# Performance work log

Hardware: AMD Instinct MI355X
Metric: run time of the kernel (lower is better)

Reference implementation:

```python
import jax, jax.numpy as jnp
from jax import lax
import numpy as np

# ---- module hyperparameters (from init_kwargs) ----
DIM = 256
DIM_HEAD = 64
HEADS = 4
GROUPS = 4                      # offset_groups (defaults to heads)
INNER = DIM_HEAD * HEADS        # 256
OFF_DIMS = INNER // GROUPS      # 64
DOWN = 4
KS = 6
PAD = (KS - DOWN) // 2          # 1
OFFSET_SCALE = float(DOWN)      # offset_scale defaults to down_sample_factor
CPB_DIM = DIM // 4              # 64
SCALE = DIM_HEAD ** -0.5


def make_grid(h, w, dtype):
    # torch.meshgrid(arange(w), arange(h), indexing='xy') stacked at dim 0:
    # channel 0 = x (column index), channel 1 = y (row index); shape [2,h,w]
    yy, xx = jnp.meshgrid(jnp.arange(h), jnp.arange(w), indexing='ij')
    return jnp.stack([xx, yy], axis=0).astype(dtype)


def normalize_grid_c(vg):
    # vg: [..., 2, h, w] -> [..., h, w, 2]; faithful to source: channel 0
    # normalized by (h-1), channel 1 by (w-1) (source's h/w naming quirk).
    h, w = vg.shape[-2:]
    gh = 2.0 * vg[..., 0, :, :] / max(h - 1, 1) - 1.0
    gw = 2.0 * vg[..., 1, :, :] / max(w - 1, 1) - 1.0
    return jnp.stack([gh, gw], axis=-1)


def grid_sample_zeros(img, grid):
    # F.grid_sample bilinear, padding_mode='zeros', align_corners=False
    # img: [N,C,H,W]; grid: [N,Hg,Wg,2] with (..,0)=x, (..,1)=y in [-1,1]
    N, C, H, W = img.shape
    ix = ((grid[..., 0] + 1.0) * W - 1.0) * 0.5
    iy = ((grid[..., 1] + 1.0) * H - 1.0) * 0.5
    x0 = jnp.floor(ix)
    y0 = jnp.floor(iy)

    def gather(yy, xx):
        valid = (xx >= 0) & (xx <= W - 1) & (yy >= 0) & (yy <= H - 1)
        xc = jnp.clip(xx, 0, W - 1).astype(jnp.int32)
        yc = jnp.clip(yy, 0, H - 1).astype(jnp.int32)
        vals = jax.vmap(lambda im, y_, x_: im[:, y_, x_])(img, yc, xc)  # [N,C,Hg,Wg]
        return vals * valid[:, None, :, :].astype(img.dtype)

    wa = (x0 + 1 - ix) * (y0 + 1 - iy)
    wb = (ix - x0) * (y0 + 1 - iy)
    wc = (x0 + 1 - ix) * (iy - y0)
    wd = (ix - x0) * (iy - y0)
    return (gather(y0, x0) * wa[:, None]
            + gather(y0, x0 + 1) * wb[:, None]
            + gather(y0 + 1, x0) * wc[:, None]
            + gather(y0 + 1, x0 + 1) * wd[:, None])


def gconv1x1(t, w):
    # grouped 1x1 conv (no bias): t [b, G*Ci, h, w], w [G, Co, Ci]
    G, Co, Ci = w.shape
    bb, _, hh, ww = t.shape
    tg = t.reshape(bb, G, Ci, hh, ww)
    return jnp.einsum('bgihw,goi->bgohw', tg, w).reshape(bb, G * Co, hh, ww)


def setup_inputs() -> dict:
    key = jax.random.key(0)
    ks = jax.random.split(key, 12)
    s = 0.02
    B, H, W = 8, 32, 32
    cg = DIM // GROUPS  # per-group in-channels = 64
    og = INNER // GROUPS  # per-group out-channels = 64
    return {
        'x': jax.random.normal(ks[0], (B, DIM, H, W), jnp.float32),
        'wq': jax.random.normal(ks[1], (GROUPS, og, cg), jnp.float32) * s,
        'wk': jax.random.normal(ks[2], (GROUPS, og, cg), jnp.float32) * s,
        'wv': jax.random.normal(ks[3], (GROUPS, og, cg), jnp.float32) * s,
        'w_off_dw': jax.random.normal(ks[4], (OFF_DIMS, 1, KS, KS), jnp.float32) * s,
        'b_off_dw': jnp.zeros((OFF_DIMS,), jnp.float32),
        'w_off_pw': jax.random.normal(ks[5], (2, OFF_DIMS), jnp.float32) * s,
        'cpb_w1': jax.random.normal(ks[6], (CPB_DIM, 2), jnp.float32) * s,
        'cpb_b1': jnp.zeros((CPB_DIM,), jnp.float32),
        'cpb_w2': jax.random.normal(ks[7], (CPB_DIM, CPB_DIM), jnp.float32) * s,
        'cpb_b2': jnp.zeros((CPB_DIM,), jnp.float32),
        'cpb_w3': jax.random.normal(ks[8], (HEADS // GROUPS, CPB_DIM), jnp.float32) * s,
        'cpb_b3': jnp.zeros((HEADS // GROUPS,), jnp.float32),
        'w_out': jax.random.normal(ks[9], (DIM, INNER), jnp.float32) * s,
        'b_out': jnp.zeros((DIM,), jnp.float32),
    }


def reference(x, wq, wk, wv, w_off_dw, b_off_dw, w_off_pw,
              cpb_w1, cpb_b1, cpb_w2, cpb_b2, cpb_w3, cpb_b3,
              w_out, b_out):
    b, _, H, W = x.shape

    q = gconv1x1(x, wq)                                       # [b, INNER, H, W]
    gq = q.reshape(b * GROUPS, OFF_DIMS, H, W)                # grouped queries
    gx = x.reshape(b * GROUPS, DIM // GROUPS, H, W)           # grouped input

    # to_offsets: depthwise conv -> GELU -> 1x1 conv -> tanh -> scale
    off = lax.conv_general_dilated(
        gq, w_off_dw, window_strides=(DOWN, DOWN),
        padding=[(PAD, PAD), (PAD, PAD)],
        dimension_numbers=('NCHW', 'OIHW', 'NCHW'),
        feature_group_count=OFF_DIMS)
    off = off + b_off_dw[None, :, None, None]
    off = jax.nn.gelu(off, approximate=False)
    off = jnp.einsum('bchw,oc->bohw', off, w_off_pw)
    off = jnp.tanh(off) * OFFSET_SCALE                        # [bg, 2, h2, w2]

    h2, w2 = off.shape[-2:]
    vg = make_grid(h2, w2, off.dtype)[None] + off             # [bg, 2, h2, w2]
    vgs = normalize_grid_c(vg)                                # [bg, h2, w2, 2]

    kv = grid_sample_zeros(gx, vgs)                           # [bg, DIM/G, h2, w2]
    kv = kv.reshape(b, DIM, h2, w2)
    k = gconv1x1(kv, wk)
    v = gconv1x1(kv, wv)
    q = q * SCALE

    def to_heads(t):
        bb, _, hh, ww = t.shape
        return t.reshape(bb, HEADS, DIM_HEAD, hh * ww).transpose(0, 1, 3, 2)

    qh, kh, vh = to_heads(q), to_heads(k), to_heads(v)        # [b, h, i|j, d]
    sim = jnp.einsum('bhid,bhjd->bhij', qh, kh)               # [b, h, HW, h2*w2]

    # CPB relative position bias
    grid_q = normalize_grid_c(make_grid(H, W, x.dtype)).reshape(1, H * W, 2)
    grid_kv = vgs.reshape(b * GROUPS, h2 * w2, 2)
    pos = grid_q[:, :, None, :] - grid_kv[:, None, :, :]      # [bg, i, j, 2]
    bias = jnp.sign(pos) * jnp.log1p(jnp.abs(pos))
    bias = jax.nn.relu(bias @ cpb_w1.T + cpb_b1)
    bias = jax.nn.relu(bias @ cpb_w2.T + cpb_b2)
    bias = bias @ cpb_w3.T + cpb_b3                           # [bg, i, j, o]
    o = HEADS // GROUPS
    bias = bias.reshape(b, GROUPS, H * W, h2 * w2, o)
    bias = bias.transpose(0, 1, 4, 2, 3).reshape(b, HEADS, H * W, h2 * w2)

    attn = jax.nn.softmax(sim + bias, axis=-1)
    out = jnp.einsum('bhij,bhjd->bhid', attn, vh)             # [b, h, HW, d]
    out = out.transpose(0, 1, 3, 2).reshape(b, INNER, H, W)
    out = jnp.einsum('bchw,oc->bohw', out, w_out) + b_out[None, :, None, None]
    return out
```

## Files before the change

kernel.cpp:

```cpp
#include <hip/hip_runtime.h>
#include <hip/hip_bf16.h>
#include <math.h>

#define QSCALE 0.125f

typedef __attribute__((ext_vector_type(8))) short short8b;
typedef __attribute__((ext_vector_type(8))) _Float16 half8;
typedef __attribute__((ext_vector_type(4))) float f32x4;

__device__ __forceinline__ uint pack2(float a, float b) {
    uint r;
    asm("v_cvt_pk_bf16_f32 %0, %1, %2" : "=v"(r) : "v"(a), "v"(b));
    return r;
}
__device__ __forceinline__ uint pkrtz(float a, float b) {
    uint r;
    asm("v_cvt_pkrtz_f16_f32 %0, %1, %2" : "=v"(r) : "v"(a), "v"(b));
    return r;
}
__device__ __forceinline__ uint pk_fma_f16(uint a, uint b, uint c) {
    uint r;
    asm("v_pk_fma_f16 %0, %1, %2, %3" : "=v"(r) : "v"(a), "v"(b), "v"(c));
    return r;
}
__device__ __forceinline__ uint pk_max_f16(uint a, uint b) {
    uint r;
    asm("v_pk_max_f16 %0, %1, %2" : "=v"(r) : "v"(a), "v"(b));
    return r;
}
__device__ __forceinline__ float slogf_(float p) {
    return copysignf(log1pf(fabsf(p)), p);
}

__global__ __launch_bounds__(256) void k_qproj(const float* __restrict__ x,
                                               const float* __restrict__ wq,
                                               float* __restrict__ q,
                                               short* __restrict__ qbt) {
    __shared__ float Wst[64 * 64];
    __shared__ float xs[64 * 128];
    int ht = blockIdx.x, g = blockIdx.y, b = blockIdx.z;
    int tid = threadIdx.x;
    for (int e = tid; e < 4096; e += 256) {
        int co = e >> 6, ci = e & 63;
        Wst[ci * 64 + co] = wq[(g * 64 + co) * 64 + ci];
    }
    const float* xb = x + (b * 256 + g * 64) * 1024 + ht * 128;
    for (int e = tid; e < 2048; e += 256) {
        int ci = e >> 5, hq = e & 31;
        *(float4*)&xs[ci * 128 + hq * 4] = *(const float4*)&xb[ci * 1024 + hq * 4];
    }
    __syncthreads();
    int cg = tid >> 4, hg = tid & 15;
    int co0 = cg * 4, hw0 = hg * 8;
    float acc[4][8];
    for (int a = 0; a < 4; a++) for (int c = 0; c < 8; c++) acc[a][c] = 0.f;
    for (int ci = 0; ci < 64; ci++) {
        float4 a4 = *(float4*)&Wst[ci * 64 + co0];
        float4 b0 = *(float4*)&xs[ci * 128 + hw0];
        float4 b1 = *(float4*)&xs[ci * 128 + hw0 + 4];
        float av[4] = {a4.x, a4.y, a4.z, a4.w};
        float bv[8] = {b0.x, b0.y, b0.z, b0.w, b1.x, b1.y, b1.z, b1.w};
        #pragma unroll
        for (int a = 0; a < 4; a++)
            #pragma unroll
            for (int c = 0; c < 8; c++) acc[a][c] += av[a] * bv[c];
    }
    float* qb = q + (b * 256 + g * 64) * 1024 + ht * 128;
    for (int a = 0; a < 4; a++) {
        float4 o0 = {acc[a][0], acc[a][1], acc[a][2], acc[a][3]};
        float4 o1 = {acc[a][4], acc[a][5], acc[a][6], acc[a][7]};
        *(float4*)&qb[(co0 + a) * 1024 + hw0] = o0;
        *(float4*)&qb[(co0 + a) * 1024 + hw0 + 4] = o1;
    }
    short* q16 = qbt + ((size_t)((b * 4 + g) * 1024 + ht * 128)) * 64;
    for (int c = 0; c < 8; c++) {
        int i = hw0 + c;
        uint2 uu;
        uu.x = pack2(acc[0][c] * QSCALE, acc[1][c] * QSCALE);
        uu.y = pack2(acc[2][c] * QSCALE, acc[3][c] * QSCALE);
        *(uint2*)&q16[i * 64 + co0] = uu;
    }
}

__global__ __launch_bounds__(256) void k_dw(const float* __restrict__ q,
                                            const float* __restrict__ wdw,
                                            const float* __restrict__ bdw,
                                            float* __restrict__ gdw) {
    __shared__ float qs[8 * 1024];
    __shared__ float wds[8 * 36];
    int cg = blockIdx.x, n = blockIdx.y;
    int b = n >> 2, gg = n & 3;
    int c0 = cg * 8;
    int tid = threadIdx.x;
    const float* qn = q + (b * 256 + gg * 64 + c0) * 1024;
    for (int e = tid; e < 2048; e += 256)
        ((float4*)qs)[e] = ((const float4*)qn)[e];
    for (int e = tid; e < 288; e += 256)
        wds[e] = wdw[c0 * 36 + e];
    __syncthreads();
    for (int e = tid; e < 512; e += 256) {
        int c = e >> 6, pos = e & 63;
        int oy = pos >> 3, ox = pos & 7;
        float acc = bdw[c0 + c];
        #pragma unroll
        for (int ky = 0; ky < 6; ky++) {
            int iy = oy * 4 - 1 + ky;
            if (iy < 0 || iy > 31) continue;
            #pragma unroll
            for (int kx = 0; kx < 6; kx++) {
                int ix = ox * 4 - 1 + kx;
                if (ix < 0 || ix > 31) continue;
                acc += qs[c * 1024 + iy * 32 + ix] * wds[c * 36 + ky * 6 + kx];
            }
        }
        gdw[(n * 64 + c0 + c) * 64 + pos] = acc * 0.5f * (1.f + erff(acc * 0.70710678118654752f));
    }
}

__global__ __launch_bounds__(64) void k_pw(const float* __restrict__ gdw,
                                           const float* __restrict__ wpw,
                                           float* __restrict__ vgs) {
    int n = blockIdx.x, pos = threadIdx.x;
    const float* gp = gdw + n * 4096 + pos;
    float a0 = 0.f, a1 = 0.f;
    #pragma unroll 8
    for (int c = 0; c < 64; c++) {
        float v = gp[c * 64];
        a0 += v * wpw[c];
        a1 += v * wpw[64 + c];
    }
    float offx = tanhf(a0) * 4.0f, offy = tanhf(a1) * 4.0f;
    int oy = pos >> 3, ox = pos & 7;
    vgs[(n * 64 + pos) * 2]     = 2.f * ((float)ox + offx) / 7.f - 1.f;
    vgs[(n * 64 + pos) * 2 + 1] = 2.f * ((float)oy + offy) / 7.f - 1.f;
}

__global__ __launch_bounds__(256) void k_sample(const float* __restrict__ x,
                                                const float* __restrict__ vgs,
                                                float* __restrict__ kv) {
    int idx = blockIdx.x * 256 + threadIdx.x;
    int pos = idx & 63, c = (idx >> 6) & 63, n = idx >> 12;
    int b = n >> 2, g = n & 3;
    float gx = vgs[(n * 64 + pos) * 2];
    float gy = vgs[(n * 64 + pos) * 2 + 1];
    float ix = (gx + 1.f) * 16.f - 0.5f;
    float iy = (gy + 1.f) * 16.f - 0.5f;
    float x0 = floorf(ix), y0 = floorf(iy);
    float wa = (x0 + 1.f - ix) * (y0 + 1.f - iy);
    float wb = (ix - x0) * (y0 + 1.f - iy);
    float wc = (x0 + 1.f - ix) * (iy - y0);
    float wd = (ix - x0) * (iy - y0);
    const float* img = x + (b * 256 + g * 64 + c) * 1024;
    int xi = (int)x0, yi = (int)y0;
    float acc = 0.f;
    if (xi >= 0 && xi <= 31 && yi >= 0 && yi <= 31)         acc += img[yi * 32 + xi] * wa;
    if (xi + 1 >= 0 && xi + 1 <= 31 && yi >= 0 && yi <= 31) acc += img[yi * 32 + xi + 1] * wb;
    if (xi >= 0 && xi <= 31 && yi + 1 >= 0 && yi + 1 <= 31) acc += img[(yi + 1) * 32 + xi] * wc;
    if (xi + 1 >= 0 && xi + 1 <= 31 && yi + 1 >= 0 && yi + 1 <= 31) acc += img[(yi + 1) * 32 + xi + 1] * wd;
    kv[(n * 64 + c) * 64 + pos] = acc;
}

__global__ __launch_bounds__(256) void k_kvproj(const float* __restrict__ kv,
                                                const float* __restrict__ wk,
                                                const float* __restrict__ wv,
                                                short* __restrict__ kob,
                                                short* __restrict__ vob) {
    __shared__ float kvs[4096];
    __shared__ float wkt[4096];
    __shared__ float wvt[4096];
    int n = blockIdx.x, g = n & 3;
    int tid = threadIdx.x;
    for (int e = tid; e < 4096; e += 256) {
        int co = e >> 6, ci = e & 63;
        wkt[ci * 64 + co] = wk[(g * 64 + co) * 64 + ci];
        wvt[ci * 64 + co] = wv[(g * 64 + co) * 64 + ci];
        kvs[e] = kv[n * 4096 + e];
    }
    __syncthreads();
    int cg = tid >> 4, jg = tid & 15;
    int co0 = cg * 4, j0 = jg * 4;
    float ak[4][4] = {}, av[4][4] = {};
    for (int ci = 0; ci < 64; ci++) {
        float4 a1 = *(float4*)&wkt[ci * 64 + co0];
        float4 a2 = *(float4*)&wvt[ci * 64 + co0];
        float4 b4 = *(float4*)&kvs[ci * 64 + j0];
        float w1v[4] = {a1.x, a1.y, a1.z, a1.w};
        float w2v[4] = {a2.x, a2.y, a2.z, a2.w};
        float bb[4] = {b4.x, b4.y, b4.z, b4.w};
        #pragma unroll
        for (int a = 0; a < 4; a++)
            #pragma unroll
            for (int j = 0; j < 4; j++) { ak[a][j] += w1v[a] * bb[j]; av[a][j] += w2v[a] * bb[j]; }
    }
    for (int jj = 0; jj < 4; jj++) {
        uint2 uu;
        uu.x = pack2(ak[0][jj], ak[1][jj]);
        uu.y = pack2(ak[2][jj], ak[3][jj]);
        *(uint2*)&kob[n * 4096 + (j0 + jj) * 64 + co0] = uu;
    }
    for (int a = 0; a < 4; a++) {
        uint2 uu;
        uu.x = pack2(av[a][0], av[a][1]);
        uu.y = pack2(av[a][2], av[a][3]);
        *(uint2*)&vob[n * 4096 + (co0 + a) * 64 + j0] = uu;
    }
}

__global__ __launch_bounds__(256) void k_wcvt(const float* __restrict__ w,
                                              short* __restrict__ wb) {
    int e = (blockIdx.x * 256 + threadIdx.x) * 8;
    float4 f0 = *(const float4*)&w[e];
    float4 f1 = *(const float4*)&w[e + 4];
    uint4 u = {pack2(f0.x, f0.y), pack2(f0.z, f0.w), pack2(f1.x, f1.y), pack2(f1.z, f1.w)};
    *(uint4*)&wb[e] = u;
}

__global__ __launch_bounds__(256) void k_cpb(const float* __restrict__ vgs,
                                             const float* __restrict__ w1,
                                             const float* __restrict__ b1,
                                             const float* __restrict__ w2,
                                             const float* __restrict__ b2,
                                             const float* __restrict__ w3,
                                             const float* __restrict__ b3,
                                             float* __restrict__ bias) {
    __shared__ uint Q1p[64 * 36];
    __shared__ uint u0p[32 * 64];
    __shared__ float u1t[64];
    int iy = blockIdx.x, n = blockIdx.y, tid = threadIdx.x;
    float qy = 2.f * (float)iy / 31.f - 1.f;

    if (tid < 64) u1t[tid] = slogf_(qy - vgs[(n << 7) + tid * 2 + 1]);
    __syncthreads();
    for (int e = tid; e < 2048; e += 256) {
        int j = e >> 5, pp = e & 31;
        int k = pp * 2;
        float lo = fmaf(w1[2 * k + 1], u1t[j], b1[k]);
        float hi = fmaf(w1[2 * k + 3], u1t[j], b1[k + 1]);
        Q1p[j * 36 + pp] = pkrtz(lo, hi);
    }
    for (int e = tid; e < 2048; e += 256) {
        int ix = e >> 6, j = e & 63;
        float qx = (2.f / 31.f) * (float)ix - 1.f;
        float u = slogf_(qx - vgs[(n << 7) + j * 2]);
        u0p[e] = pkrtz(u, u);
    }

    int wid = tid >> 6, lane = tid & 63, lr = lane & 15, g = lane >> 4;
    float b3v = b3[0];

    half8 w2f[4][2];
    #pragma unroll
    for (int m = 0; m < 4; m++)
        #pragma unroll
        for (int s = 0; s < 2; s++) {
            const float* wp = w2 + (m * 16 + lr) * 64 + s * 32 + g * 8;
            float4 c0 = *(const float4*)wp;
            float4 c1 = *(const float4*)(wp + 4);
            uint4 uu = {pkrtz(c0.x, c0.y), pkrtz(c0.z, c0.w),
                        pkrtz(c1.x, c1.y), pkrtz(c1.z, c1.w)};
            w2f[m][s] = __builtin_bit_cast(half8, uu);
        }
    uint w1ap[2][4];
    #pragma unroll
    for (int s = 0; s < 2; s++)
        #pragma unroll
        for (int p = 0; p < 4; p++) {
            int k = s * 32 + g * 8 + 2 * p;
            w1ap[s][p] = pkrtz(w1[2 * k], w1[2 * k + 2]);
        }
    float w3r[4][4], b2r[4][4];
    #pragma unroll
    for (int m = 0; m < 4; m++)
        #pragma unroll
        for (int r = 0; r < 4; r++) {
            int c2 = m * 16 + g * 4 + r;
            w3r[m][r] = w3[c2];
            b2r[m][r] = b2[c2];
        }
    uint zero16 = 0;
    __syncthreads();

    for (int ii = 0; ii < 8; ii++) {
        int ix = wid * 8 + ii;
        int iG = iy * 32 + ix;
        float outv = 0.f;
        #pragma unroll
        for (int ntH = 0; ntH < 2; ntH++) {
            half8 bf[2][2];
            #pragma unroll
            for (int ntl = 0; ntl < 2; ntl++) {
                int nt = ntH * 2 + ntl;
                uint u0v = u0p[ix * 64 + nt * 16 + lr];
                const uint* q1p = &Q1p[(nt * 16 + lr) * 36];
                #pragma unroll
                for (int s = 0; s < 2; s++) {
                    uint4 q4 = *(const uint4*)&q1p[s * 16 + g * 4];
                    uint4 hb;
                    hb.x = pk_max_f16(pk_fma_f16(w1ap[s][0], u0v, q4.x), zero16);
                    hb.y = pk_max_f16(pk_fma_f16(w1ap[s][1], u0v, q4.y), zero16);
                    hb.z = pk_max_f16(pk_fma_f16(w1ap[s][2], u0v, q4.z), zero16);
                    hb.w = pk_max_f16(pk_fma_f16(w1ap[s][3], u0v, q4.w), zero16);
                    bf[ntl][s] = __builtin_bit_cast(half8, hb);
                }
            }
            f32x4 acc[4][2];
            #pragma unroll
            for (int m = 0; m < 4; m++)
                #pragma unroll
                for (int l = 0; l < 2; l++)
                    acc[m][l] = (f32x4){b2r[m][0], b2r[m][1], b2r[m][2], b2r[m][3]};
            #pragma unroll
            for (int s = 0; s < 2; s++)
                #pragma unroll
                for (int m = 0; m < 4; m++)
                    #pragma unroll
                    for (int l = 0; l < 2; l++)
                        acc[m][l] = __builtin_amdgcn_mfma_f32_16x16x32_f16(
                            w2f[m][s], bf[l][s], acc[m][l], 0, 0, 0);
            float t0 = 0.f, t1 = 0.f;
            #pragma unroll
            for (int m = 0; m < 4; m++)
                #pragma unroll
                for (int r = 0; r < 4; r++) {
                    t0 += w3r[m][r] * fmaxf(acc[m][0][r], 0.f);
                    t1 += w3r[m][r] * fmaxf(acc[m][1][r], 0.f);
                }
            t0 += __shfl_xor(t0, 16); t0 += __shfl_xor(t0, 32);
            t1 += __shfl_xor(t1, 16); t1 += __shfl_xor(t1, 32);
            if ((g >> 1) == ntH) outv = (g & 1) ? t1 : t0;
        }
        bias[((size_t)n * 1024 + iG) * 64 + lane] = outv + b3v;
    }
}

__global__ __launch_bounds__(256) void k_attn(const short* __restrict__ qbt,
                                              const short* __restrict__ kob,
                                              const short* __restrict__ vob,
                                              const float* __restrict__ bias,
                                              short* __restrict__ attb) {
    __shared__ float scr[4][1088];
    int it = blockIdx.x, h = blockIdx.y, b = blockIdx.z;
    int n = b * 4 + h;
    int tid = threadIdx.x, wid = tid >> 6, lane = tid & 63, lr = lane & 15, g = lane >> 4;
    int i0w = it * 64 + wid * 16;
    float* P = scr[wid];

    const short* kb = kob + n * 4096;
    short8b kf[4][2];
    #pragma unroll
    for (int nt = 0; nt < 4; nt++)
        #pragma unroll
        for (int s = 0; s < 2; s++)
            kf[nt][s] = *(const short8b*)&kb[(nt * 16 + lr) * 64 + s * 32 + g * 8];
    const short* vb = vob + n * 4096;
    short8b vf[4][2];
    #pragma unroll
    for (int nt = 0; nt < 4; nt++)
        #pragma unroll
        for (int s = 0; s < 2; s++)
            vf[nt][s] = *(const short8b*)&vb[(nt * 16 + lr) * 64 + s * 32 + g * 8];
    const short* qb = qbt + ((size_t)n * 1024 + i0w + lr) * 64;
    short8b qf[2];
    qf[0] = *(const short8b*)&qb[g * 8];
    qf[1] = *(const short8b*)&qb[32 + g * 8];
    float bv[4][4];
    #pragma unroll
    for (int r = 0; r < 4; r++)
        #pragma unroll
        for (int nt = 0; nt < 4; nt++)
            bv[r][nt] = bias[((size_t)n * 1024 + i0w + g * 4 + r) * 64 + nt * 16 + lr];

    f32x4 acc[4];
    #pragma unroll
    for (int nt = 0; nt < 4; nt++) acc[nt] = (f32x4){0.f, 0.f, 0.f, 0.f};
    #pragma unroll
    for (int s = 0; s < 2; s++)
        #pragma unroll
        for (int nt = 0; nt < 4; nt++)
            acc[nt] = __builtin_amdgcn_mfma_f32_16x16x32_bf16(qf[s], kf[nt][s], acc[nt], 0, 0, 0);

    #pragma unroll
    for (int r = 0; r < 4; r++) {
        float s0 = acc[0][r] + bv[r][0], s1 = acc[1][r] + bv[r][1];
        float s2 = acc[2][r] + bv[r][2], s3 = acc[3][r] + bv[r][3];
        float m = fmaxf(fmaxf(s0, s1), fmaxf(s2, s3));
        m = fmaxf(m, __shfl_xor(m, 1));
        m = fmaxf(m, __shfl_xor(m, 2));
        m = fmaxf(m, __shfl_xor(m, 4));
        m = fmaxf(m, __shfl_xor(m, 8));
        float e0 = __expf(s0 - m), e1 = __expf(s1 - m);
        float e2 = __expf(s2 - m), e3 = __expf(s3 - m);
        float sum = (e0 + e1) + (e2 + e3);
        sum += __shfl_xor(sum, 1);
        sum += __shfl_xor(sum, 2);
        sum += __shfl_xor(sum, 4);
        sum += __shfl_xor(sum, 8);
        float inv = 1.f / sum;
        int row = g * 4 + r;
        P[row * 68 + lr]      = e0 * inv;
        P[row * 68 + 16 + lr] = e1 * inv;
        P[row * 68 + 32 + lr] = e2 * inv;
        P[row * 68 + 48 + lr] = e3 * inv;
    }

    const float* pr = &P[lr * 68];
    float4 a0 = *(float4*)&pr[g * 8];
    float4 a1 = *(float4*)&pr[g * 8 + 4];
    float4 a2 = *(float4*)&pr[32 + g * 8];
    float4 a3 = *(float4*)&pr[32 + g * 8 + 4];
    uint4 up0 = {pack2(a0.x, a0.y), pack2(a0.z, a0.w), pack2(a1.x, a1.y), pack2(a1.z, a1.w)};
    uint4 up1 = {pack2(a2.x, a2.y), pack2(a2.z, a2.w), pack2(a3.x, a3.y), pack2(a3.z, a3.w)};
    short8b pf0 = __builtin_bit_cast(short8b, up0);
    short8b pf1 = __builtin_bit_cast(short8b, up1);

    f32x4 oacc[4];
    #pragma unroll
    for (int nt = 0; nt < 4; nt++) oacc[nt] = (f32x4){0.f, 0.f, 0.f, 0.f};
    #pragma unroll
    for (int nt = 0; nt < 4; nt++) {
        oacc[nt] = __builtin_amdgcn_mfma_f32_16x16x32_bf16(pf0, vf[nt][0], oacc[nt], 0, 0, 0);
        oacc[nt] = __builtin_amdgcn_mfma_f32_16x16x32_bf16(pf1, vf[nt][1], oacc[nt], 0, 0, 0);
    }

    #pragma unroll
    for (int nt = 0; nt < 4; nt++)
        #pragma unroll
        for (int r = 0; r < 4; r++)
            P[(nt * 16 + lr) * 17 + g * 4 + r] = oacc[nt][r];
    int il = lane >> 2, dq = lane & 3;
    uint ub[8];
    #pragma unroll
    for (int t = 0; t < 8; t++) {
        float lo = P[(dq * 16 + 2 * t) * 17 + il];
        float hi = P[(dq * 16 + 2 * t + 1) * 17 + il];
        ub[t] = pack2(lo, hi);
    }
    short* op = attb + ((size_t)(b * 1024 + i0w + il)) * 256 + h * 64 + dq * 16;
    uint4 s0v = {ub[0], ub[1], ub[2], ub[3]};
    uint4 s1v = {ub[4], ub[5], ub[6], ub[7]};
    ((uint4*)op)[0] = s0v;
    ((uint4*)op)[1] = s1v;
}

__global__ __launch_bounds__(256) void k_outproj(const short* __restrict__ attb,
                                                 const short* __restrict__ wob,
                                                 const float* __restrict__ bout,
                                                 float* __restrict__ y) {
    int rt = blockIdx.x;
    int ct = blockIdx.y;
    int tid = threadIdx.x, wid = tid >> 6, lane = tid & 63, lr = lane & 15, g = lane >> 4;
    int wr = wid >> 1, wc = wid & 1;
    int b = rt >> 5;
    int hw0 = (rt & 31) * 32 + wr * 16;
    int cobase = ct * 128 + wc * 64;
    const short* arow = attb + ((size_t)(b * 1024) + hw0) * 256;
    const short* brow = wob + (size_t)cobase * 256;

    f32x4 acc[4];
    #pragma unroll
    for (int nn = 0; nn < 4; nn++) acc[nn] = (f32x4){0.f, 0.f, 0.f, 0.f};
    #pragma unroll
    for (int s = 0; s < 8; s++) {
        short8b af = *(const short8b*)&arow[lr * 256 + s * 32 + g * 8];
        #pragma unroll
        for (int nn = 0; nn < 4; nn++) {
            short8b bf = *(const short8b*)&brow[(nn * 16 + lr) * 256 + s * 32 + g * 8];
            acc[nn] = __builtin_amdgcn_mfma_f32_16x16x32_bf16(af, bf, acc[nn], 0, 0, 0);
        }
    }
    #pragma unroll
    for (int nn = 0; nn < 4; nn++) {
        int co = cobase + nn * 16 + lr;
        float bo = bout[co];
        float4 o = {acc[nn][0] + bo, acc[nn][1] + bo, acc[nn][2] + bo, acc[nn][3] + bo};
        *(float4*)&y[(size_t)b * 262144 + (size_t)co * 1024 + hw0 + g * 4] = o;
    }
}

extern "C" void kernel_launch(void* const* d_in, const int* in_sizes, int n_in,
                              void* d_out, int out_size, void* d_ws, size_t ws_size,
                              hipStream_t stream) {
    const float* x    = (const float*)d_in[0];
    const float* wq   = (const float*)d_in[1];
    const float* wk   = (const float*)d_in[2];
    const float* wv   = (const float*)d_in[3];
    const float* wdw  = (const float*)d_in[4];
    const float* bdw  = (const float*)d_in[5];
    const float* wpw  = (const float*)d_in[6];
    const float* cw1  = (const float*)d_in[7];
    const float* cb1  = (const float*)d_in[8];
    const float* cw2  = (const float*)d_in[9];
    const float* cb2  = (const float*)d_in[10];
    const float* cw3  = (const float*)d_in[11];
    const float* cb3  = (const float*)d_in[12];
    const float* wout = (const float*)d_in[13];
    const float* bout = (const float*)d_in[14];
    float* y  = (float*)d_out;
    float* ws = (float*)d_ws;

    float* q    = ws;
    short* attb = (short*)ws;
    float* bias = ws + 2097152;
    float* kv   = ws + 4194304;
    float* vgs  = ws + 4325376;
    short* qbt  = (short*)(ws + 4329472);
    short* kob  = (short*)(ws + 5378048);
    short* vob  = (short*)(ws + 5443584);
    float* gdw  = ws + 5509120;
    short* wob  = (short*)(ws + 5640192);

    k_qproj  <<<dim3(8, 4, 8),  256, 0, stream>>>(x, wq, q, qbt);
    k_wcvt   <<<32,             256, 0, stream>>>(wout, wob);
    k_dw     <<<dim3(8, 32),    256, 0, stream>>>(q, wdw, bdw, gdw);
    k_pw     <<<32,              64, 0, stream>>>(gdw, wpw, vgs);
    k_sample <<<512,            256, 0, stream>>>(x, vgs, kv);
    k_kvproj <<<32,             256, 0, stream>>>(kv, wk, wv, kob, vob);
    k_cpb    <<<dim3(32, 32),   256, 0, stream>>>(vgs, cw1, cb1, cw2, cb2, cw3, cb3, bias);
    k_attn   <<<dim3(16, 4, 8), 256, 0, stream>>>(qbt, kob, vob, bias, attb);
    k_outproj<<<dim3(256, 2),   256, 0, stream>>>(attb, wob, bout, y);
}
```

Baseline: 103.9 us.

## Split CPB blocks over x halves and precompute x-log table in separate kernel

The CPB kernel's grid doubles so each block handles half a row of query x positions, which raises block count and parallelism. The per-column signed-log x table is computed once by a new small kernel into global memory instead of being recomputed in every block. The bias is now folded into the first MFMA's accumulator input. In exchange there is one extra kernel launch, and each block still recomputes the Q1p table, so that setup work is duplicated across twice as many blocks.

After: 107.5 us. 3.4% more time.

```diff
diff --git a/kernel.cpp b/kernel.cpp
--- a/kernel.cpp
+++ b/kernel.cpp
@@ -133,6 +133,17 @@
     int oy = pos >> 3, ox = pos & 7;
     vgs[(n * 64 + pos) * 2]     = 2.f * ((float)ox + offx) / 7.f - 1.f;
     vgs[(n * 64 + pos) * 2 + 1] = 2.f * ((float)oy + offy) / 7.f - 1.f;
+}
+
+__global__ __launch_bounds__(256) void k_u0(const float* __restrict__ vgs,
+                                            uint* __restrict__ u0g) {
+    int n = blockIdx.x, tid = threadIdx.x;
+    for (int e = tid; e < 2048; e += 256) {
+        int ix = e >> 6, j = e & 63;
+        float qx = (2.f / 31.f) * (float)ix - 1.f;
+        float u = slogf_(qx - vgs[(n << 7) + j * 2]);
+        u0g[n * 2048 + e] = pkrtz(u, u);
+    }
 }
 
 __global__ __launch_bounds__(256) void k_sample(const float* __restrict__ x,
@@ -216,6 +227,7 @@
 }
 
 __global__ __launch_bounds__(256) void k_cpb(const float* __restrict__ vgs,
+                                             const uint* __restrict__ u0g,
                                              const float* __restrict__ w1,
                                              const float* __restrict__ b1,
                                              const float* __restrict__ w2,
@@ -224,9 +236,9 @@
                                              const float* __restrict__ b3,
                                              float* __restrict__ bias) {
     __shared__ uint Q1p[64 * 36];
-    __shared__ uint u0p[32 * 64];
+    __shared__ uint u0p[16 * 64];
     __shared__ float u1t[64];
-    int iy = blockIdx.x, n = blockIdx.y, tid = threadIdx.x;
+    int iy = blockIdx.x >> 1, xh = blockIdx.x & 1, n = blockIdx.y, tid = threadIdx.x;
     float qy = 2.f * (float)iy / 31.f - 1.f;
 
     if (tid < 64) u1t[tid] = slogf_(qy - vgs[(n << 7) + tid * 2 + 1]);
@@ -238,12 +250,8 @@
         float hi = fmaf(w1[2 * k + 3], u1t[j], b1[k + 1]);
         Q1p[j * 36 + pp] = pkrtz(lo, hi);
     }
-    for (int e = tid; e < 2048; e += 256) {
-        int ix = e >> 6, j = e & 63;
-        float qx = (2.f / 31.f) * (float)ix - 1.f;
-        float u = slogf_(qx - vgs[(n << 7) + j * 2]);
-        u0p[e] = pkrtz(u, u);
-    }
+    for (int e = tid; e < 1024; e += 256)
+        u0p[e] = u0g[n * 2048 + xh * 1024 + e];
 
     int wid = tid >> 6, lane = tid & 63, lr = lane & 15, g = lane >> 4;
     float b3v = b3[0];
@@ -268,21 +276,22 @@
             int k = s * 32 + g * 8 + 2 * p;
             w1ap[s][p] = pkrtz(w1[2 * k], w1[2 * k + 2]);
         }
-    float w3r[4][4], b2r[4][4];
+    float w3r[4][4];
+    f32x4 b2v[4];
     #pragma unroll
     for (int m = 0; m < 4; m++)
         #pragma unroll
         for (int r = 0; r < 4; r++) {
             int c2 = m * 16 + g * 4 + r;
             w3r[m][r] = w3[c2];
-            b2r[m][r] = b2[c2];
+            b2v[m][r] = b2[c2];
         }
     uint zero16 = 0;
     __syncthreads();
 
-    for (int ii = 0; ii < 8; ii++) {
-        int ix = wid * 8 + ii;
-        int iG = iy * 32 + ix;
+    for (int ii = 0; ii < 4; ii++) {
+        int ixl = wid * 4 + ii;
+        int iG = iy * 32 + xh * 16 + ixl;
         float outv = 0.f;
         #pragma unroll
         for (int ntH = 0; ntH < 2; ntH++) {
@@ -290,7 +299,7 @@
             #pragma unroll
             for (int ntl = 0; ntl < 2; ntl++) {
                 int nt = ntH * 2 + ntl;
-                uint u0v = u0p[ix * 64 + nt * 16 + lr];
+                uint u0v = u0p[ixl * 64 + nt * 16 + lr];
                 const uint* q1p = &Q1p[(nt * 16 + lr) * 36];
                 #pragma unroll
                 for (int s = 0; s < 2; s++) {
@@ -308,15 +317,14 @@
             for (int m = 0; m < 4; m++)
                 #pragma unroll
                 for (int l = 0; l < 2; l++)
-                    acc[m][l] = (f32x4){b2r[m][0], b2r[m][1], b2r[m][2], b2r[m][3]};
-            #pragma unroll
-            for (int s = 0; s < 2; s++)
+                    acc[m][l] = __builtin_amdgcn_mfma_f32_16x16x32_f16(
+                        w2f[m][0], bf[l][0], b2v[m], 0, 0, 0);
+            #pragma unroll
+            for (int m = 0; m < 4; m++)
                 #pragma unroll
-                for (int m = 0; m < 4; m++)
-                    #pragma unroll
-                    for (int l = 0; l < 2; l++)
-                        acc[m][l] = __builtin_amdgcn_mfma_f32_16x16x32_f16(
-                            w2f[m][s], bf[l][s], acc[m][l], 0, 0, 0);
+                for (int l = 0; l < 2; l++)
+                    acc[m][l] = __builtin_amdgcn_mfma_f32_16x16x32_f16(
+                        w2f[m][1], bf[l][1], acc[m][l], 0, 0, 0);
             float t0 = 0.f, t1 = 0.f;
             #pragma unroll
             for (int m = 0; m < 4; m++)
@@ -508,14 +516,16 @@
     short* vob  = (short*)(ws + 5443584);
     float* gdw  = ws + 5509120;
     short* wob  = (short*)(ws + 5640192);
+    uint*  u0g  = (uint*)(ws + 5672960);
 
     k_qproj  <<<dim3(8, 4, 8),  256, 0, stream>>>(x, wq, q, qbt);
     k_wcvt   <<<32,             256, 0, stream>>>(wout, wob);
     k_dw     <<<dim3(8, 32),    256, 0, stream>>>(q, wdw, bdw, gdw);
     k_pw     <<<32,              64, 0, stream>>>(gdw, wpw, vgs);
+    k_u0     <<<32,             256, 0, stream>>>(vgs, u0g);
     k_sample <<<512,            256, 0, stream>>>(x, vgs, kv);
     k_kvproj <<<32,             256, 0, stream>>>(kv, wk, wv, kob, vob);
-    k_cpb    <<<dim3(32, 32),   256, 0, stream>>>(vgs, cw1, cb1, cw2, cb2, cw3, cb3, bias);
+    k_cpb    <<<dim3(64, 32),   256, 0, stream>>>(vgs, u0g, cw1, cb1, cw2, cb2, cw3, cb3, bias);
     k_attn   <<<dim3(16, 4, 8), 256, 0, stream>>>(qbt, kob, vob, bias, attb);
     k_outproj<<<dim3(256, 2),   256, 0, stream>>>(attb, wob, bout, y);
 }
```
